# Kernel tuning notes

Measured on AMD Instinct MI355X. Metric: run time of the kernel, lower is better.

Reference implementation:

```python
import jax, jax.numpy as jnp
import numpy as np

B, T, D, H, Dh = 2, 2048, 2048, 16, 128


def setup_inputs() -> dict:
    key = jax.random.key(0)
    ks = jax.random.split(key, 9)
    s = 0.02
    return {
        "x": jax.random.normal(ks[0], (B, T, D), jnp.float32),
        "Wq": jax.random.normal(ks[1], (H, D, Dh), jnp.float32) * s,
        "bq": jax.random.normal(ks[2], (H, Dh), jnp.float32) * s,
        "Wk": jax.random.normal(ks[3], (H, D, Dh), jnp.float32) * s,
        "bk": jax.random.normal(ks[4], (H, Dh), jnp.float32) * s,
        "Wv": jax.random.normal(ks[5], (H, D, Dh), jnp.float32) * s,
        "bv": jax.random.normal(ks[6], (H, Dh), jnp.float32) * s,
        "Wp": jax.random.normal(ks[7], (D, D), jnp.float32) * s,
        "bp": jax.random.normal(ks[8], (D,), jnp.float32) * s,
    }


def reference(x, Wq, bq, Wk, bk, Wv, bv, Wp, bp):
    # per-head projections (stacked): [B, H, T, Dh]
    q = jnp.einsum("btd,hde->bhte", x, Wq) + bq[None, :, None, :]
    k = jnp.einsum("btd,hde->bhte", x, Wk) + bk[None, :, None, :]
    v = jnp.einsum("btd,hde->bhte", x, Wv) + bv[None, :, None, :]
    scale = Dh ** -0.5
    att = jnp.einsum("bhte,bhse->bhts", q, k) * scale  # [B,H,T,T]
    causal = jnp.tril(jnp.ones((T, T), bool))
    att = jnp.where(causal, att, -jnp.inf)
    att = jax.nn.softmax(att, axis=-1)
    # dropout p=0.0 -> identity
    out = jnp.einsum("bhts,bhse->bhte", att, v)  # [B,H,T,Dh]
    out = out.transpose(0, 2, 1, 3).reshape(B, T, H * Dh)  # concat heads
    return out @ Wp.T if False else jnp.einsum("btd,ed->bte", out, Wp.T) if False else out @ Wp + bp
```

## Files before the change

kernel.cpp:

```cpp
#include <hip/hip_runtime.h>
#include <hip/hip_bf16.h>
#include <math.h>

typedef __attribute__((ext_vector_type(8))) short bf16x8;
typedef __attribute__((ext_vector_type(4))) float f32x4;

__device__ __forceinline__ unsigned short f2b(float f) {
    union { float f; unsigned u; } a; a.f = f;
    unsigned r = a.u + 0x7FFFu + ((a.u >> 16) & 1u);
    return (unsigned short)(r >> 16);
}

__device__ __forceinline__ void gl_lds16(const unsigned short* g, unsigned short* l) {
    __builtin_amdgcn_global_load_lds(
        (const __attribute__((address_space(1))) unsigned int*)g,
        (__attribute__((address_space(3))) unsigned int*)l,
        16, 0, 0);
}

__global__ __launch_bounds__(256) void cast_x_kernel(const float* __restrict__ x,
                                                     unsigned short* __restrict__ xb, int n4) {
    int i = blockIdx.x * 256 + threadIdx.x;
    if (i >= n4) return;
    float4 v = ((const float4*)x)[i];
    ushort4 o;
    o.x = f2b(v.x); o.y = f2b(v.y); o.z = f2b(v.z); o.w = f2b(v.w);
    ((ushort4*)xb)[i] = o;
}

__global__ __launch_bounds__(256) void transpose_cast_kernel(const float* __restrict__ in,
                                                             unsigned short* __restrict__ out,
                                                             int R, int C) {
    __shared__ float tile[32][33];
    size_t mo = (size_t)blockIdx.z * R * C;
    const float* src = in + mo;
    unsigned short* dst = out + mo;
    int c0 = blockIdx.x * 32, r0 = blockIdx.y * 32;
    int tx = threadIdx.x, ty = threadIdx.y;
#pragma unroll
    for (int i = 0; i < 32; i += 8)
        tile[ty + i][tx] = src[(size_t)(r0 + ty + i) * C + c0 + tx];
    __syncthreads();
#pragma unroll
    for (int i = 0; i < 32; i += 8)
        dst[(size_t)(c0 + ty + i) * R + r0 + tx] = f2b(tile[tx][ty + i]);
}

constexpr int BKg = 64;

__global__ __launch_bounds__(256) void qkv_gemm_kernel(
    const unsigned short* __restrict__ xb,
    const unsigned short* __restrict__ wt,
    const float* __restrict__ bq, const float* __restrict__ bkb, const float* __restrict__ bvb,
    unsigned short* __restrict__ q, unsigned short* __restrict__ k, unsigned short* __restrict__ vt) {
    __shared__ unsigned short sA[128 * 64];
    __shared__ unsigned short sB[128 * 64];
    int cb = blockIdx.x;
    int m0 = blockIdx.y * 128;
    int tid = threadIdx.x;
    int lane = tid & 63, w = tid >> 6;
    int wm = w >> 1, wn = w & 1;
    int ln = lane & 15, quad = lane >> 4;
    int srow = lane >> 3;
    int gcol = ((lane & 7) ^ srow) * 8;
    int swz = ln & 7;

    f32x4 acc[4][4] = {};
    const unsigned short* aBase = xb + (size_t)m0 * 2048;
    const unsigned short* bBase = wt + (size_t)cb * 128 * 2048;

    for (int k0 = 0; k0 < 2048; k0 += BKg) {
#pragma unroll
        for (int p = 0; p < 4; ++p) {
            int row = w * 32 + p * 8 + srow;
            gl_lds16(aBase + (size_t)row * 2048 + k0 + gcol, sA + (w * 32 + p * 8) * 64);
            gl_lds16(bBase + (size_t)row * 2048 + k0 + gcol, sB + (w * 32 + p * 8) * 64);
        }
        __syncthreads();
#pragma unroll
        for (int ks = 0; ks < 2; ++ks) {
            bf16x8 af[4], bfr[4];
#pragma unroll
            for (int i = 0; i < 4; ++i)
                af[i] = *(const bf16x8*)(sA + (wm * 64 + i * 16 + ln) * 64 + ((ks * 4 + quad) ^ swz) * 8);
#pragma unroll
            for (int i = 0; i < 4; ++i)
                bfr[i] = *(const bf16x8*)(sB + (wn * 64 + i * 16 + ln) * 64 + ((ks * 4 + quad) ^ swz) * 8);
#pragma unroll
            for (int i = 0; i < 4; ++i)
#pragma unroll
                for (int j = 0; j < 4; ++j)
                    acc[i][j] = __builtin_amdgcn_mfma_f32_16x16x32_bf16(af[i], bfr[j], acc[i][j], 0, 0, 0);
        }
        __syncthreads();
    }

    int mat = cb >> 4, h = cb & 15;
    const float* bias = (mat == 0) ? bq : (mat == 1) ? bkb : bvb;
    unsigned short* outqk = (mat == 0) ? q : k;
#pragma unroll
    for (int i = 0; i < 4; ++i) {
#pragma unroll
        for (int j = 0; j < 4; ++j) {
            int e = wn * 64 + j * 16 + ln;
            float bb = bias[h * 128 + e];
            if (mat < 2) {
#pragma unroll
                for (int r = 0; r < 4; ++r) {
                    int gr = m0 + wm * 64 + i * 16 + quad * 4 + r;
                    int b = gr >> 11, t = gr & 2047;
                    outqk[((size_t)(b * 16 + h) * 2048 + t) * 128 + e] = f2b(acc[i][j][r] + bb);
                }
            } else {
                int gr = m0 + wm * 64 + i * 16 + quad * 4;
                int b = gr >> 11, t = gr & 2047;
                ushort4 pk;
                pk.x = f2b(acc[i][j][0] + bb);
                pk.y = f2b(acc[i][j][1] + bb);
                pk.z = f2b(acc[i][j][2] + bb);
                pk.w = f2b(acc[i][j][3] + bb);
                *(ushort4*)(vt + ((size_t)(b * 16 + h) * 128 + e) * 2048 + t) = pk;
            }
        }
    }
}

__global__ __launch_bounds__(256) void attn_kernel(
    const unsigned short* __restrict__ qg,
    const unsigned short* __restrict__ kg,
    const unsigned short* __restrict__ vg,
    unsigned short* __restrict__ og) {
    constexpr int LDP = 72;
    __shared__ unsigned short sK[64 * 128];
    __shared__ unsigned short sV[128 * 64];
    __shared__ unsigned short sP[4 * 32 * LDP];

    int bh = blockIdx.x;
    int t0 = (15 - (int)blockIdx.y) * 128;
    int tid = threadIdx.x;
    int lane = tid & 63, w = tid >> 6;
    int ln = lane & 15, quad = lane >> 4;
    int swz = ln & 7;

    const unsigned short* qb = qg + (size_t)bh * 2048 * 128;
    const unsigned short* kb = kg + (size_t)bh * 2048 * 128;
    const unsigned short* vb = vg + (size_t)bh * 128 * 2048;

    bf16x8 qf[2][4];
#pragma unroll
    for (int i = 0; i < 2; ++i)
#pragma unroll
        for (int c = 0; c < 4; ++c)
            qf[i][c] = *(const bf16x8*)(qb + (size_t)(t0 + w * 32 + i * 16 + ln) * 128 + c * 32 + quad * 8);

    f32x4 oacc[2][8] = {};
    float mst[2][4], lst[2][4];
#pragma unroll
    for (int i = 0; i < 2; ++i)
#pragma unroll
        for (int r = 0; r < 4; ++r) { mst[i][r] = -INFINITY; lst[i][r] = 0.f; }

    int wtmax = t0 + w * 32 + 31;
    int nblk = (t0 + 128) / 64;
    const float scale = 0.08838834764831845f;

    int kr = lane >> 4, km = lane & 15;
    int vr = lane >> 3, vm = lane & 7;

    for (int jb = 0; jb < nblk; ++jb) {
        int s0 = jb * 64;
#pragma unroll
        for (int p = 0; p < 4; ++p) {
            int krow = w * 16 + p * 4;
            int rswk = (krow + kr) & 7;
            int kch = (km & 8) | ((km & 7) ^ rswk);
            gl_lds16(kb + (size_t)(s0 + krow + kr) * 128 + kch * 8, sK + krow * 128);
            int vrow = w * 32 + p * 8;
            int vch = vm ^ vr;
            gl_lds16(vb + (size_t)(vrow + vr) * 2048 + s0 + vch * 8, sV + vrow * 64);
        }
        __syncthreads();
        if (s0 <= wtmax) {
            f32x4 sacc[2][4] = {};
#pragma unroll
            for (int c = 0; c < 4; ++c) {
                bf16x8 bfr[4];
#pragma unroll
                for (int j = 0; j < 4; ++j) {
                    int ch = c * 4 + quad;
                    int pos = (ch & 8) | ((ch ^ swz) & 7);
                    bfr[j] = *(const bf16x8*)(sK + (j * 16 + ln) * 128 + pos * 8);
                }
#pragma unroll
                for (int i = 0; i < 2; ++i)
#pragma unroll
                    for (int j = 0; j < 4; ++j)
                        sacc[i][j] = __builtin_amdgcn_mfma_f32_16x16x32_bf16(qf[i][c], bfr[j], sacc[i][j], 0, 0, 0);
            }
#pragma unroll
            for (int i = 0; i < 2; ++i) {
#pragma unroll
                for (int r = 0; r < 4; ++r) {
                    int t = t0 + w * 32 + i * 16 + quad * 4 + r;
                    float pv[4];
                    float rm = -INFINITY;
#pragma unroll
                    for (int j = 0; j < 4; ++j) {
                        int s = s0 + j * 16 + ln;
                        float vv = sacc[i][j][r] * scale;
                        if (s > t) vv = -INFINITY;
                        pv[j] = vv;
                        rm = fmaxf(rm, vv);
                    }
#pragma unroll
                    for (int m_ = 8; m_ >= 1; m_ >>= 1)
                        rm = fmaxf(rm, __shfl_xor(rm, m_, 64));
                    float mnew = fmaxf(mst[i][r], rm);
                    float alpha = __expf(mst[i][r] - mnew);
                    float rsum = 0.f;
#pragma unroll
                    for (int j = 0; j < 4; ++j) {
                        float p_ = __expf(pv[j] - mnew);
                        rsum += p_;
                        sP[(w * 32 + i * 16 + quad * 4 + r) * LDP + j * 16 + ln] = f2b(p_);
                    }
#pragma unroll
                    for (int m_ = 8; m_ >= 1; m_ >>= 1)
                        rsum += __shfl_xor(rsum, m_, 64);
                    lst[i][r] = lst[i][r] * alpha + rsum;
                    mst[i][r] = mnew;
#pragma unroll
                    for (int jj = 0; jj < 8; ++jj)
                        oacc[i][jj][r] *= alpha;
                }
            }
#pragma unroll
            for (int c2_ = 0; c2_ < 2; ++c2_) {
                bf16x8 af[2], bfr[8];
#pragma unroll
                for (int i = 0; i < 2; ++i)
                    af[i] = *(const bf16x8*)(sP + (w * 32 + i * 16 + ln) * LDP + c2_ * 32 + quad * 8);
#pragma unroll
                for (int jj = 0; jj < 8; ++jj) {
                    int pos = (c2_ * 4 + quad) ^ swz;
                    bfr[jj] = *(const bf16x8*)(sV + (jj * 16 + ln) * 64 + pos * 8);
                }
#pragma unroll
                for (int i = 0; i < 2; ++i)
#pragma unroll
                    for (int jj = 0; jj < 8; ++jj)
                        oacc[i][jj] = __builtin_amdgcn_mfma_f32_16x16x32_bf16(af[i], bfr[jj], oacc[i][jj], 0, 0, 0);
            }
        }
        __syncthreads();
    }

#pragma unroll
    for (int i = 0; i < 2; ++i) {
#pragma unroll
        for (int r = 0; r < 4; ++r) {
            int t = t0 + w * 32 + i * 16 + quad * 4 + r;
            float inv = 1.f / lst[i][r];
#pragma unroll
            for (int jj = 0; jj < 8; ++jj) {
                int e = jj * 16 + ln;
                og[((size_t)bh * 2048 + t) * 128 + e] = f2b(oacc[i][jj][r] * inv);
            }
        }
    }
}

__global__ __launch_bounds__(256) void proj_gemm_kernel(
    const unsigned short* __restrict__ og,
    const unsigned short* __restrict__ wpt,
    const float* __restrict__ bp,
    float* __restrict__ out) {
    __shared__ unsigned short sA[128 * 64];
    __shared__ unsigned short sB[128 * 64];
    int cb = blockIdx.x;
    int m0 = blockIdx.y * 128;
    int b = m0 >> 11, t0_ = m0 & 2047;
    int tid = threadIdx.x;
    int lane = tid & 63, w = tid >> 6;
    int wm = w >> 1, wn = w & 1;
    int ln = lane & 15, quad = lane >> 4;
    int srow = lane >> 3;
    int gcol = ((lane & 7) ^ srow) * 8;
    int swz = ln & 7;

    f32x4 acc[4][4] = {};
    const unsigned short* bBase = wpt + (size_t)cb * 128 * 2048;

    for (int k0 = 0; k0 < 2048; k0 += BKg) {
        int h = k0 >> 7, e0 = k0 & 127;
        const unsigned short* aBase = og + ((size_t)(b * 16 + h) * 2048 + t0_) * 128 + e0;
#pragma unroll
        for (int p = 0; p < 4; ++p) {
            int row = w * 32 + p * 8 + srow;
            gl_lds16(aBase + (size_t)row * 128 + gcol, sA + (w * 32 + p * 8) * 64);
            gl_lds16(bBase + (size_t)row * 2048 + k0 + gcol, sB + (w * 32 + p * 8) * 64);
        }
        __syncthreads();
#pragma unroll
        for (int ks = 0; ks < 2; ++ks) {
            bf16x8 af[4], bfr[4];
#pragma unroll
            for (int i = 0; i < 4; ++i)
                af[i] = *(const bf16x8*)(sA + (wm * 64 + i * 16 + ln) * 64 + ((ks * 4 + quad) ^ swz) * 8);
#pragma unroll
            for (int i = 0; i < 4; ++i)
                bfr[i] = *(const bf16x8*)(sB + (wn * 64 + i * 16 + ln) * 64 + ((ks * 4 + quad) ^ swz) * 8);
#pragma unroll
            for (int i = 0; i < 4; ++i)
#pragma unroll
                for (int j = 0; j < 4; ++j)
                    acc[i][j] = __builtin_amdgcn_mfma_f32_16x16x32_bf16(af[i], bfr[j], acc[i][j], 0, 0, 0);
        }
        __syncthreads();
    }

#pragma unroll
    for (int i = 0; i < 4; ++i)
#pragma unroll
        for (int j = 0; j < 4; ++j) {
            int col = cb * 128 + wn * 64 + j * 16 + ln;
            float bias = bp[col];
#pragma unroll
            for (int r = 0; r < 4; ++r) {
                int row = m0 + wm * 64 + i * 16 + quad * 4 + r;
                out[(size_t)row * 2048 + col] = acc[i][j][r] + bias;
            }
        }
}

extern "C" void kernel_launch(void* const* d_in, const int* in_sizes, int n_in,
                              void* d_out, int out_size, void* d_ws, size_t ws_size,
                              hipStream_t stream) {
    const float* x  = (const float*)d_in[0];
    const float* Wq = (const float*)d_in[1];
    const float* bq = (const float*)d_in[2];
    const float* Wk = (const float*)d_in[3];
    const float* bk = (const float*)d_in[4];
    const float* Wv = (const float*)d_in[5];
    const float* bv = (const float*)d_in[6];
    const float* Wp = (const float*)d_in[7];
    const float* bp = (const float*)d_in[8];
    float* out = (float*)d_out;

    char* ws = (char*)d_ws;
    unsigned short* xb  = (unsigned short*)(ws);
    unsigned short* wt  = (unsigned short*)(ws + 16777216);
    unsigned short* wpt = (unsigned short*)(ws + 41943040);
    unsigned short* q   = (unsigned short*)(ws + 50331648);
    unsigned short* k   = (unsigned short*)(ws + 67108864);
    unsigned short* vt  = (unsigned short*)(ws + 83886080);
    unsigned short* o   = (unsigned short*)(ws + 100663296);

    cast_x_kernel<<<8192, 256, 0, stream>>>(x, xb, 2097152);
    dim3 tb(32, 8);
    transpose_cast_kernel<<<dim3(4, 64, 16), tb, 0, stream>>>(Wq, wt, 2048, 128);
    transpose_cast_kernel<<<dim3(4, 64, 16), tb, 0, stream>>>(Wk, wt + 16 * 128 * 2048, 2048, 128);
    transpose_cast_kernel<<<dim3(4, 64, 16), tb, 0, stream>>>(Wv, wt + 32 * 128 * 2048, 2048, 128);
    transpose_cast_kernel<<<dim3(64, 64, 1), tb, 0, stream>>>(Wp, wpt, 2048, 2048);
    qkv_gemm_kernel<<<dim3(48, 32), 256, 0, stream>>>(xb, wt, bq, bk, bv, q, k, vt);
    attn_kernel<<<dim3(32, 16), 256, 0, stream>>>(q, k, vt, o);
    proj_gemm_kernel<<<dim3(16, 32), 256, 0, stream>>>(o, wpt, bp, out);
}
```

Measured before the change: 439.3 us.

## Use 32x32 MFMA in GEMMs, shrink attention tiles, fold scale into Q

The QKV and projection GEMMs switch from 16x16x32 to 32x32x16 bf16 MFMA with 2x2 accumulators per wave, which cuts LDS fragment reads per MFMA. Attention now uses 64-query blocks with one 16-row tile per wave, doubling the grid for better load balance across the causal triangle and dropping the per-wave skip test. The softmax scale times log2(e) is folded into Q at projection time so the kernel can use exp2f with no per-element multiply. The three QKV weight transposes are merged into one launch. Smaller attention tiles reload K/V more often overall.

```diff
diff --git a/kernel.cpp b/kernel.cpp
--- a/kernel.cpp
+++ b/kernel.cpp
@@ -4,6 +4,7 @@
 
 typedef __attribute__((ext_vector_type(8))) short bf16x8;
 typedef __attribute__((ext_vector_type(4))) float f32x4;
+typedef __attribute__((ext_vector_type(16))) float f32x16;
 
 __device__ __forceinline__ unsigned short f2b(float f) {
     union { float f; unsigned u; } a; a.f = f;
@@ -17,6 +18,8 @@
         (__attribute__((address_space(3))) unsigned int*)l,
         16, 0, 0);
 }
+
+#define SCALE2 0.12751744716529944f
 
 __global__ __launch_bounds__(256) void cast_x_kernel(const float* __restrict__ x,
                                                      unsigned short* __restrict__ xb, int n4) {
@@ -32,18 +35,35 @@
                                                              unsigned short* __restrict__ out,
                                                              int R, int C) {
     __shared__ float tile[32][33];
-    size_t mo = (size_t)blockIdx.z * R * C;
-    const float* src = in + mo;
-    unsigned short* dst = out + mo;
     int c0 = blockIdx.x * 32, r0 = blockIdx.y * 32;
     int tx = threadIdx.x, ty = threadIdx.y;
 #pragma unroll
     for (int i = 0; i < 32; i += 8)
-        tile[ty + i][tx] = src[(size_t)(r0 + ty + i) * C + c0 + tx];
+        tile[ty + i][tx] = in[(size_t)(r0 + ty + i) * C + c0 + tx];
     __syncthreads();
 #pragma unroll
     for (int i = 0; i < 32; i += 8)
-        dst[(size_t)(c0 + ty + i) * R + r0 + tx] = f2b(tile[tx][ty + i]);
+        out[(size_t)(c0 + ty + i) * R + r0 + tx] = f2b(tile[tx][ty + i]);
+}
+
+__global__ __launch_bounds__(256) void transpose_cast3_kernel(const float* __restrict__ Wq,
+                                                              const float* __restrict__ Wk,
+                                                              const float* __restrict__ Wv,
+                                                              unsigned short* __restrict__ out) {
+    __shared__ float tile[32][33];
+    int z = blockIdx.z;
+    int mat = z >> 4, hh = z & 15;
+    const float* src = ((mat == 0) ? Wq : (mat == 1) ? Wk : Wv) + (size_t)hh * 2048 * 128;
+    unsigned short* dst = out + (size_t)z * 128 * 2048;
+    int c0 = blockIdx.x * 32, r0 = blockIdx.y * 32;
+    int tx = threadIdx.x, ty = threadIdx.y;
+#pragma unroll
+    for (int i = 0; i < 32; i += 8)
+        tile[ty + i][tx] = src[(size_t)(r0 + ty + i) * 128 + c0 + tx];
+    __syncthreads();
+#pragma unroll
+    for (int i = 0; i < 32; i += 8)
+        dst[(size_t)(c0 + ty + i) * 2048 + r0 + tx] = f2b(tile[tx][ty + i]);
 }
 
 constexpr int BKg = 64;
@@ -60,12 +80,12 @@
     int tid = threadIdx.x;
     int lane = tid & 63, w = tid >> 6;
     int wm = w >> 1, wn = w & 1;
-    int ln = lane & 15, quad = lane >> 4;
+    int l32 = lane & 31, kh = lane >> 5;
     int srow = lane >> 3;
     int gcol = ((lane & 7) ^ srow) * 8;
-    int swz = ln & 7;
-
-    f32x4 acc[4][4] = {};
+    int swz = l32 & 7;
+
+    f32x16 acc[2][2] = {};
     const unsigned short* aBase = xb + (size_t)m0 * 2048;
     const unsigned short* bBase = wt + (size_t)cb * 128 * 2048;
 
@@ -78,19 +98,20 @@
         }
         __syncthreads();
 #pragma unroll
-        for (int ks = 0; ks < 2; ++ks) {
-            bf16x8 af[4], bfr[4];
-#pragma unroll
-            for (int i = 0; i < 4; ++i)
-                af[i] = *(const bf16x8*)(sA + (wm * 64 + i * 16 + ln) * 64 + ((ks * 4 + quad) ^ swz) * 8);
-#pragma unroll
-            for (int i = 0; i < 4; ++i)
-                bfr[i] = *(const bf16x8*)(sB + (wn * 64 + i * 16 + ln) * 64 + ((ks * 4 + quad) ^ swz) * 8);
-#pragma unroll
-            for (int i = 0; i < 4; ++i)
-#pragma unroll
-                for (int j = 0; j < 4; ++j)
-                    acc[i][j] = __builtin_amdgcn_mfma_f32_16x16x32_bf16(af[i], bfr[j], acc[i][j], 0, 0, 0);
+        for (int kst = 0; kst < 4; ++kst) {
+            int chunk = kst * 2 + kh;
+            bf16x8 af[2], bfr[2];
+#pragma unroll
+            for (int a = 0; a < 2; ++a)
+                af[a] = *(const bf16x8*)(sA + (wm * 64 + a * 32 + l32) * 64 + (chunk ^ swz) * 8);
+#pragma unroll
+            for (int b = 0; b < 2; ++b)
+                bfr[b] = *(const bf16x8*)(sB + (wn * 64 + b * 32 + l32) * 64 + (chunk ^ swz) * 8);
+#pragma unroll
+            for (int a = 0; a < 2; ++a)
+#pragma unroll
+                for (int b = 0; b < 2; ++b)
+                    acc[a][b] = __builtin_amdgcn_mfma_f32_32x32x16_bf16(af[a], bfr[b], acc[a][b], 0, 0, 0);
         }
         __syncthreads();
     }
@@ -98,28 +119,33 @@
     int mat = cb >> 4, h = cb & 15;
     const float* bias = (mat == 0) ? bq : (mat == 1) ? bkb : bvb;
     unsigned short* outqk = (mat == 0) ? q : k;
-#pragma unroll
-    for (int i = 0; i < 4; ++i) {
-#pragma unroll
-        for (int j = 0; j < 4; ++j) {
-            int e = wn * 64 + j * 16 + ln;
-            float bb = bias[h * 128 + e];
+    float postscale = (mat == 0) ? SCALE2 : 1.0f;
+#pragma unroll
+    for (int a = 0; a < 2; ++a) {
+#pragma unroll
+        for (int b = 0; b < 2; ++b) {
+            int col = wn * 64 + b * 32 + l32;
+            float bb = bias[h * 128 + col];
             if (mat < 2) {
 #pragma unroll
-                for (int r = 0; r < 4; ++r) {
-                    int gr = m0 + wm * 64 + i * 16 + quad * 4 + r;
-                    int b = gr >> 11, t = gr & 2047;
-                    outqk[((size_t)(b * 16 + h) * 2048 + t) * 128 + e] = f2b(acc[i][j][r] + bb);
+                for (int reg = 0; reg < 16; ++reg) {
+                    int gr = m0 + wm * 64 + a * 32 + (reg & 3) + 8 * (reg >> 2) + 4 * kh;
+                    int bi = gr >> 11, t = gr & 2047;
+                    outqk[((size_t)(bi * 16 + h) * 2048 + t) * 128 + col] =
+                        f2b((acc[a][b][reg] + bb) * postscale);
                 }
             } else {
-                int gr = m0 + wm * 64 + i * 16 + quad * 4;
-                int b = gr >> 11, t = gr & 2047;
-                ushort4 pk;
-                pk.x = f2b(acc[i][j][0] + bb);
-                pk.y = f2b(acc[i][j][1] + bb);
-                pk.z = f2b(acc[i][j][2] + bb);
-                pk.w = f2b(acc[i][j][3] + bb);
-                *(ushort4*)(vt + ((size_t)(b * 16 + h) * 128 + e) * 2048 + t) = pk;
+#pragma unroll
+                for (int rg = 0; rg < 4; ++rg) {
+                    int gr = m0 + wm * 64 + a * 32 + 8 * rg + 4 * kh;
+                    int bi = gr >> 11, t = gr & 2047;
+                    ushort4 pk;
+                    pk.x = f2b(acc[a][b][rg * 4 + 0] + bb);
+                    pk.y = f2b(acc[a][b][rg * 4 + 1] + bb);
+                    pk.z = f2b(acc[a][b][rg * 4 + 2] + bb);
+                    pk.w = f2b(acc[a][b][rg * 4 + 3] + bb);
+                    *(ushort4*)(vt + ((size_t)(bi * 16 + h) * 128 + col) * 2048 + t) = pk;
+                }
             }
         }
     }
@@ -133,10 +159,10 @@
     constexpr int LDP = 72;
     __shared__ unsigned short sK[64 * 128];
     __shared__ unsigned short sV[128 * 64];
-    __shared__ unsigned short sP[4 * 32 * LDP];
+    __shared__ unsigned short sP[4 * 16 * LDP];
 
     int bh = blockIdx.x;
-    int t0 = (15 - (int)blockIdx.y) * 128;
+    int t0 = (31 - (int)blockIdx.y) * 64;
     int tid = threadIdx.x;
     int lane = tid & 63, w = tid >> 6;
     int ln = lane & 15, quad = lane >> 4;
@@ -146,23 +172,17 @@
     const unsigned short* kb = kg + (size_t)bh * 2048 * 128;
     const unsigned short* vb = vg + (size_t)bh * 128 * 2048;
 
-    bf16x8 qf[2][4];
-#pragma unroll
-    for (int i = 0; i < 2; ++i)
-#pragma unroll
-        for (int c = 0; c < 4; ++c)
-            qf[i][c] = *(const bf16x8*)(qb + (size_t)(t0 + w * 32 + i * 16 + ln) * 128 + c * 32 + quad * 8);
-
-    f32x4 oacc[2][8] = {};
-    float mst[2][4], lst[2][4];
-#pragma unroll
-    for (int i = 0; i < 2; ++i)
-#pragma unroll
-        for (int r = 0; r < 4; ++r) { mst[i][r] = -INFINITY; lst[i][r] = 0.f; }
-
-    int wtmax = t0 + w * 32 + 31;
-    int nblk = (t0 + 128) / 64;
-    const float scale = 0.08838834764831845f;
+    bf16x8 qf[4];
+#pragma unroll
+    for (int c = 0; c < 4; ++c)
+        qf[c] = *(const bf16x8*)(qb + (size_t)(t0 + w * 16 + ln) * 128 + c * 32 + quad * 8);
+
+    f32x4 oacc[8] = {};
+    float mst[4], lst[4];
+#pragma unroll
+    for (int r = 0; r < 4; ++r) { mst[r] = -INFINITY; lst[r] = 0.f; }
+
+    int nblk = t0 / 64 + 1;
 
     int kr = lane >> 4, km = lane & 15;
     int vr = lane >> 3, vm = lane & 7;
@@ -180,8 +200,8 @@
             gl_lds16(vb + (size_t)(vrow + vr) * 2048 + s0 + vch * 8, sV + vrow * 64);
         }
         __syncthreads();
-        if (s0 <= wtmax) {
-            f32x4 sacc[2][4] = {};
+        {
+            f32x4 sacc[4] = {};
 #pragma unroll
             for (int c = 0; c < 4; ++c) {
                 bf16x8 bfr[4];
@@ -192,80 +212,68 @@
                     bfr[j] = *(const bf16x8*)(sK + (j * 16 + ln) * 128 + pos * 8);
                 }
 #pragma unroll
-                for (int i = 0; i < 2; ++i)
-#pragma unroll
-                    for (int j = 0; j < 4; ++j)
-                        sacc[i][j] = __builtin_amdgcn_mfma_f32_16x16x32_bf16(qf[i][c], bfr[j], sacc[i][j], 0, 0, 0);
-            }
-#pragma unroll
-            for (int i = 0; i < 2; ++i) {
-#pragma unroll
-                for (int r = 0; r < 4; ++r) {
-                    int t = t0 + w * 32 + i * 16 + quad * 4 + r;
-                    float pv[4];
-                    float rm = -INFINITY;
-#pragma unroll
-                    for (int j = 0; j < 4; ++j) {
-                        int s = s0 + j * 16 + ln;
-                        float vv = sacc[i][j][r] * scale;
-                        if (s > t) vv = -INFINITY;
-                        pv[j] = vv;
-                        rm = fmaxf(rm, vv);
-                    }
-#pragma unroll
-                    for (int m_ = 8; m_ >= 1; m_ >>= 1)
-                        rm = fmaxf(rm, __shfl_xor(rm, m_, 64));
-                    float mnew = fmaxf(mst[i][r], rm);
-                    float alpha = __expf(mst[i][r] - mnew);
-                    float rsum = 0.f;
-#pragma unroll
-                    for (int j = 0; j < 4; ++j) {
-                        float p_ = __expf(pv[j] - mnew);
-                        rsum += p_;
-                        sP[(w * 32 + i * 16 + quad * 4 + r) * LDP + j * 16 + ln] = f2b(p_);
-                    }
-#pragma unroll
-                    for (int m_ = 8; m_ >= 1; m_ >>= 1)
-                        rsum += __shfl_xor(rsum, m_, 64);
-                    lst[i][r] = lst[i][r] * alpha + rsum;
-                    mst[i][r] = mnew;
-#pragma unroll
-                    for (int jj = 0; jj < 8; ++jj)
-                        oacc[i][jj][r] *= alpha;
-                }
-            }
-#pragma unroll
-            for (int c2_ = 0; c2_ < 2; ++c2_) {
-                bf16x8 af[2], bfr[8];
-#pragma unroll
-                for (int i = 0; i < 2; ++i)
-                    af[i] = *(const bf16x8*)(sP + (w * 32 + i * 16 + ln) * LDP + c2_ * 32 + quad * 8);
+                for (int j = 0; j < 4; ++j)
+                    sacc[j] = __builtin_amdgcn_mfma_f32_16x16x32_bf16(qf[c], bfr[j], sacc[j], 0, 0, 0);
+            }
+#pragma unroll
+            for (int r = 0; r < 4; ++r) {
+                int t = t0 + w * 16 + quad * 4 + r;
+                float pv[4];
+                float rm = -INFINITY;
+#pragma unroll
+                for (int j = 0; j < 4; ++j) {
+                    int s = s0 + j * 16 + ln;
+                    float vv = sacc[j][r];
+                    if (s > t) vv = -INFINITY;
+                    pv[j] = vv;
+                    rm = fmaxf(rm, vv);
+                }
+#pragma unroll
+                for (int m_ = 8; m_ >= 1; m_ >>= 1)
+                    rm = fmaxf(rm, __shfl_xor(rm, m_, 64));
+                float mnew = fmaxf(mst[r], rm);
+                float alpha = exp2f(mst[r] - mnew);
+                float rsum = 0.f;
+#pragma unroll
+                for (int j = 0; j < 4; ++j) {
+                    float p_ = exp2f(pv[j] - mnew);
+                    rsum += p_;
+                    sP[(w * 16 + quad * 4 + r) * LDP + j * 16 + ln] = f2b(p_);
+                }
+#pragma unroll
+                for (int m_ = 8; m_ >= 1; m_ >>= 1)
+                    rsum += __shfl_xor(rsum, m_, 64);
+                lst[r] = lst[r] * alpha + rsum;
+                mst[r] = mnew;
+#pragma unroll
+                for (int jj = 0; jj < 8; ++jj)
+                    oacc[jj][r] *= alpha;
+            }
+#pragma unroll
+            for (int c2 = 0; c2 < 2; ++c2) {
+                bf16x8 af, bfr[8];
+                af = *(const bf16x8*)(sP + (w * 16 + ln) * LDP + c2 * 32 + quad * 8);
 #pragma unroll
                 for (int jj = 0; jj < 8; ++jj) {
-                    int pos = (c2_ * 4 + quad) ^ swz;
+                    int pos = (c2 * 4 + quad) ^ swz;
                     bfr[jj] = *(const bf16x8*)(sV + (jj * 16 + ln) * 64 + pos * 8);
                 }
 #pragma unroll
-                for (int i = 0; i < 2; ++i)
-#pragma unroll
-                    for (int jj = 0; jj < 8; ++jj)
-                        oacc[i][jj] = __builtin_amdgcn_mfma_f32_16x16x32_bf16(af[i], bfr[jj], oacc[i][jj], 0, 0, 0);
-            }
-        }
-        __syncthreads();
-    }
-
-#pragma unroll
-    for (int i = 0; i < 2; ++i) {
-#pragma unroll
-        for (int r = 0; r < 4; ++r) {
-            int t = t0 + w * 32 + i * 16 + quad * 4 + r;
-            float inv = 1.f / lst[i][r];
-#pragma unroll
-            for (int jj = 0; jj < 8; ++jj) {
-                int e = jj * 16 + ln;
-                og[((size_t)bh * 2048 + t) * 128 + e] = f2b(oacc[i][jj][r] * inv);
-            }
+                for (int jj = 0; jj < 8; ++jj)
+                    oacc[jj] = __builtin_amdgcn_mfma_f32_16x16x32_bf16(af, bfr[jj], oacc[jj], 0, 0, 0);
+            }
+        }
+        __syncthreads();
+    }
+
+#pragma unroll
+    for (int r = 0; r < 4; ++r) {
+        int t = t0 + w * 16 + quad * 4 + r;
+        float inv = 1.f / lst[r];
+#pragma unroll
+        for (int jj = 0; jj < 8; ++jj) {
+            int e = jj * 16 + ln;
+            og[((size_t)bh * 2048 + t) * 128 + e] = f2b(oacc[jj][r] * inv);
         }
     }
 }
@@ -279,21 +287,21 @@
     __shared__ unsigned short sB[128 * 64];
     int cb = blockIdx.x;
     int m0 = blockIdx.y * 128;
-    int b = m0 >> 11, t0_ = m0 & 2047;
+    int b_ = m0 >> 11, t0_ = m0 & 2047;
     int tid = threadIdx.x;
     int lane = tid & 63, w = tid >> 6;
     int wm = w >> 1, wn = w & 1;
-    int ln = lane & 15, quad = lane >> 4;
+    int l32 = lane & 31, kh = lane >> 5;
     int srow = lane >> 3;
     int gcol = ((lane & 7) ^ srow) * 8;
-    int swz = ln & 7;
-
-    f32x4 acc[4][4] = {};
+    int swz = l32 & 7;
+
+    f32x16 acc[2][2] = {};
     const unsigned short* bBase = wpt + (size_t)cb * 128 * 2048;
 
     for (int k0 = 0; k0 < 2048; k0 += BKg) {
         int h = k0 >> 7, e0 = k0 & 127;
-        const unsigned short* aBase = og + ((size_t)(b * 16 + h) * 2048 + t0_) * 128 + e0;
+        const unsigned short* aBase = og + ((size_t)(b_ * 16 + h) * 2048 + t0_) * 128 + e0;
 #pragma unroll
         for (int p = 0; p < 4; ++p) {
             int row = w * 32 + p * 8 + srow;
@@ -302,33 +310,34 @@
         }
         __syncthreads();
 #pragma unroll
-        for (int ks = 0; ks < 2; ++ks) {
-            bf16x8 af[4], bfr[4];
-#pragma unroll
-            for (int i = 0; i < 4; ++i)
-                af[i] = *(const bf16x8*)(sA + (wm * 64 + i * 16 + ln) * 64 + ((ks * 4 + quad) ^ swz) * 8);
-#pragma unroll
-            for (int i = 0; i < 4; ++i)
-                bfr[i] = *(const bf16x8*)(sB + (wn * 64 + i * 16 + ln) * 64 + ((ks * 4 + quad) ^ swz) * 8);
-#pragma unroll
-            for (int i = 0; i < 4; ++i)
-#pragma unroll
-                for (int j = 0; j < 4; ++j)
-                    acc[i][j] = __builtin_amdgcn_mfma_f32_16x16x32_bf16(af[i], bfr[j], acc[i][j], 0, 0, 0);
-        }
-        __syncthreads();
-    }
-
-#pragma unroll
-    for (int i = 0; i < 4; ++i)
-#pragma unroll
-        for (int j = 0; j < 4; ++j) {
-            int col = cb * 128 + wn * 64 + j * 16 + ln;
+        for (int kst = 0; kst < 4; ++kst) {
+            int chunk = kst * 2 + kh;
+            bf16x8 af[2], bfr[2];
+#pragma unroll
+            for (int a = 0; a < 2; ++a)
+                af[a] = *(const bf16x8*)(sA + (wm * 64 + a * 32 + l32) * 64 + (chunk ^ swz) * 8);
+#pragma unroll
+            for (int b = 0; b < 2; ++b)
+                bfr[b] = *(const bf16x8*)(sB + (wn * 64 + b * 32 + l32) * 64 + (chunk ^ swz) * 8);
+#pragma unroll
+            for (int a = 0; a < 2; ++a)
+#pragma unroll
+                for (int b = 0; b < 2; ++b)
+                    acc[a][b] = __builtin_amdgcn_mfma_f32_32x32x16_bf16(af[a], bfr[b], acc[a][b], 0, 0, 0);
+        }
+        __syncthreads();
+    }
+
+#pragma unroll
+    for (int a = 0; a < 2; ++a)
+#pragma unroll
+        for (int b = 0; b < 2; ++b) {
+            int col = cb * 128 + wn * 64 + b * 32 + l32;
             float bias = bp[col];
 #pragma unroll
-            for (int r = 0; r < 4; ++r) {
-                int row = m0 + wm * 64 + i * 16 + quad * 4 + r;
-                out[(size_t)row * 2048 + col] = acc[i][j][r] + bias;
+            for (int reg = 0; reg < 16; ++reg) {
+                int row = m0 + wm * 64 + a * 32 + (reg & 3) + 8 * (reg >> 2) + 4 * kh;
+                out[(size_t)row * 2048 + col] = acc[a][b][reg] + bias;
             }
         }
 }
@@ -358,11 +367,9 @@
 
     cast_x_kernel<<<8192, 256, 0, stream>>>(x, xb, 2097152);
     dim3 tb(32, 8);
-    transpose_cast_kernel<<<dim3(4, 64, 16), tb, 0, stream>>>(Wq, wt, 2048, 128);
-    transpose_cast_kernel<<<dim3(4, 64, 16), tb, 0, stream>>>(Wk, wt + 16 * 128 * 2048, 2048, 128);
-    transpose_cast_kernel<<<dim3(4, 64, 16), tb, 0, stream>>>(Wv, wt + 32 * 128 * 2048, 2048, 128);
+    transpose_cast3_kernel<<<dim3(4, 64, 48), tb, 0, stream>>>(Wq, Wk, Wv, wt);
     transpose_cast_kernel<<<dim3(64, 64, 1), tb, 0, stream>>>(Wp, wpt, 2048, 2048);
     qkv_gemm_kernel<<<dim3(48, 32), 256, 0, stream>>>(xb, wt, bq, bk, bv, q, k, vt);
-    attn_kernel<<<dim3(32, 16), 256, 0, stream>>>(q, k, vt, o);
+    attn_kernel<<<dim3(32, 32), 256, 0, stream>>>(q, k, vt, o);
     proj_gemm_kernel<<<dim3(16, 32), 256, 0, stream>>>(o, wpt, bp, out);
 }
```

After: 413.0 us. 6.0% less time.
